# Performance work log

Measured on AMD Instinct MI355X. Metric: run time of the kernel, lower is better.

## Reference

```python
import jax, jax.numpy as jnp
import numpy as np

B, T, E, H, LBL = 32, 2048, 256, 256, 20


def _lstm_cell_step(x, W_ih, b_ih, b_hh):
    # Single LSTM cell step from zero state (h0=c0=0): W_hh @ h0 == 0.
    # x: [B, T, E]; W_ih: [4H, E]; gate order in torch: i, f, g, o
    gates = jnp.einsum('bte,ge->btg', x, W_ih) + b_ih + b_hh  # [B, T, 4H]
    i, f, g, o = jnp.split(gates, 4, axis=-1)
    c = jax.nn.sigmoid(i) * jnp.tanh(g)  # f * c0 == 0
    return jax.nn.sigmoid(o) * jnp.tanh(c)  # [B, T, H]


def setup_inputs() -> dict:
    key = jax.random.key(0)
    ks = jax.random.split(key, 12)
    s_ih = 1.0 / np.sqrt(H)
    inp = {
        'X': jax.random.normal(ks[0], (B, T, E), dtype=jnp.float32),
        'lengths': jax.random.randint(ks[1], (B,), 1, T + 1, dtype=jnp.int32),
        'W_ih_f': jax.random.uniform(ks[2], (4 * H, E), jnp.float32, -s_ih, s_ih),
        'b_ih_f': jax.random.uniform(ks[3], (4 * H,), jnp.float32, -s_ih, s_ih),
        'b_hh_f': jax.random.uniform(ks[4], (4 * H,), jnp.float32, -s_ih, s_ih),
        'W_ih_r': jax.random.uniform(ks[5], (4 * H, E), jnp.float32, -s_ih, s_ih),
        'b_ih_r': jax.random.uniform(ks[6], (4 * H,), jnp.float32, -s_ih, s_ih),
        'b_hh_r': jax.random.uniform(ks[7], (4 * H,), jnp.float32, -s_ih, s_ih),
        'W1': jax.random.uniform(ks[8], (256, 4 * H), jnp.float32, -1 / np.sqrt(4 * H), 1 / np.sqrt(4 * H)),
        'b1': jax.random.uniform(ks[9], (256,), jnp.float32, -1 / np.sqrt(4 * H), 1 / np.sqrt(4 * H)),
        'W2': jax.random.uniform(ks[10], (LBL, 256), jnp.float32, -1 / 16.0, 1 / 16.0),
        'b2': jax.random.uniform(ks[11], (LBL,), jnp.float32, -1 / 16.0, 1 / 16.0),
    }
    return inp


def reference(X, lengths, W_ih_f, b_ih_f, b_hh_f, W_ih_r, b_ih_r, b_hh_r, W1, b1, W2, b2):
    lengths = jnp.clip(lengths, 1, T).astype(jnp.int32)
    # Both directions are independent single-step cells (seq_len==1 in original)
    h_f = _lstm_cell_step(X, W_ih_f, b_ih_f, b_hh_f)  # [B, T, H]
    h_r = _lstm_cell_step(X, W_ih_r, b_ih_r, b_hh_r)  # [B, T, H]
    s = jnp.concatenate([h_f, h_r], axis=-1)          # [B, T, 2H]
    mask = (jnp.arange(T)[None, :] < lengths[:, None])  # [B, T]
    m = mask[:, :, None].astype(s.dtype)
    avg_pool = (s * m).sum(axis=1) / lengths[:, None].astype(s.dtype)  # [B, 2H]
    NEG = jnp.asarray(-1e30, s.dtype)
    max_pool = jnp.where(mask[:, :, None], s, NEG).max(axis=1)          # [B, 2H]
    doc = jnp.concatenate([avg_pool, max_pool], axis=-1)                # [B, 4H]
    rel = jax.nn.relu(doc)
    d1 = rel @ W1.T + b1        # dropout is identity in eval mode
    return d1 @ W2.T + b2        # [B, LBL]
```

## Files before the change

kernel.cpp:

```cpp
#include <hip/hip_runtime.h>
#include <stdint.h>

#define B_   32
#define T_   2048
#define E_   256
#define H_   256
#define LBL_ 20
#define M_   (B_ * T_)
#define NPACK_ 1536

typedef __attribute__((ext_vector_type(8))) short bf16x8;
typedef __attribute__((ext_vector_type(4))) float f32x4;

__device__ __forceinline__ unsigned short f2bf(float f) {
    union { float f; unsigned int u; } a; a.f = f;
    unsigned int u = a.u;
    u += 0x7FFFu + ((u >> 16) & 1u);
    return (unsigned short)(u >> 16);
}

__device__ __forceinline__ float rcp_(float x) {
#if __has_builtin(__builtin_amdgcn_rcpf)
    return __builtin_amdgcn_rcpf(x);
#else
    return 1.0f / x;
#endif
}
__device__ __forceinline__ float exp2_(float x) {
#if __has_builtin(__builtin_amdgcn_exp2f)
    return __builtin_amdgcn_exp2f(x);
#else
    return exp2f(x);
#endif
}

__global__ __launch_bounds__(256) void prep(
    const float4* __restrict__ X4, uint4* __restrict__ Xb4,
    const int* __restrict__ lengths,
    const float* __restrict__ Wf, const float* __restrict__ bif, const float* __restrict__ bhf,
    const float* __restrict__ Wr, const float* __restrict__ bir, const float* __restrict__ bhr,
    unsigned short* __restrict__ Wp, float* __restrict__ bias_p,
    int* __restrict__ live)
{
    int bi = blockIdx.x;
    if (bi < 8192) {
        int b = bi >> 8, tile = bi & 255;
        int lenb = lengths[b]; lenb = lenb < 1 ? 1 : (lenb > T_ ? T_ : lenb);
        int used = (lenb + 127) & ~127;
        if (tile * 8 >= used) return;
        int idx = b * 65536 + tile * 256 + threadIdx.x;
        float4 v0 = X4[2 * idx], v1 = X4[2 * idx + 1];
        union { unsigned short us[8]; uint4 u; } r;
        r.us[0] = f2bf(v0.x); r.us[1] = f2bf(v0.y); r.us[2] = f2bf(v0.z); r.us[3] = f2bf(v0.w);
        r.us[4] = f2bf(v1.x); r.us[5] = f2bf(v1.y); r.us[6] = f2bf(v1.z); r.us[7] = f2bf(v1.w);
        Xb4[idx] = r.u;
    } else if (bi < 8192 + NPACK_) {
        int n = bi - 8192, t = threadIdx.x;
        int gidx = n / 48, r = n % 48;
        int ty = r >> 4, cc = r & 15;
        int dir = gidx >> 4, c = (gidx & 15) * 16 + cc;
        int gate = (ty == 0) ? 0 : (ty == 1 ? 2 : 3);
        int wrow = gate * 256 + c;
        const float* W = dir ? Wr : Wf;
        Wp[n * 256 + t] = f2bf(W[wrow * 256 + t]);
        if (t == 0)
            bias_p[n] = (dir ? bir[wrow] : bif[wrow]) + (dir ? bhr[wrow] : bhf[wrow]);
    } else {
        __shared__ int cnts[32], offs[32], lens[32];
        int t = threadIdx.x;
        if (t < 32) {
            int lenb = lengths[t]; lenb = lenb < 1 ? 1 : (lenb > T_ ? T_ : lenb);
            lens[t] = lenb;
            cnts[t] = (lenb + 127) >> 7;
        }
        __syncthreads();
        if (t == 0) {
            int acc = 0;
            for (int b = 0; b < 32; ++b) { offs[b] = acc; acc += cnts[b]; }
            live[0] = acc;
        }
        __syncthreads();
        if (t < 32) {
            int o = offs[t], lenb = lens[t];
            for (int k = 0; k < cnts[t]; ++k)
                live[1 + o + k] = (lenb << 9) | (t * 16 + k);
        }
    }
}

__global__ __launch_bounds__(256, 3) void gemm_pool(
    const unsigned short* __restrict__ Xb, const unsigned short* __restrict__ Wp,
    const float* __restrict__ bias_p, const int* __restrict__ live,
    float* __restrict__ psum, float* __restrict__ pmax)
{
    __shared__ __align__(16) short Bs[96 * 256];
    __shared__ float red[2][4][2][16][2];

    const int tid    = threadIdx.x;
    const int w      = tid >> 6;
    const int lane   = tid & 63;
    const int n_tile = blockIdx.x / 48;
    const int worker = blockIdx.x % 48;
    const int n0     = n_tile * 96;
    const int q      = lane >> 4;
    const int cc     = lane & 15;

    #pragma unroll
    for (int rr = 0; rr < 12; ++rr) {
        int s = rr * 256 + tid;
        int row = s >> 5, kcs = s & 31;
        int kc = (kcs & 24) | ((kcs & 7) ^ (row & 7));
        __builtin_amdgcn_global_load_lds(
            (const __attribute__((address_space(1))) void*)(Wp + (n0 + row) * 256 + kc * 8),
            (__attribute__((address_space(3))) void*)(Bs + (rr * 256 + (w << 6)) * 8),
            16, 0, 0);
    }

    float bI[2], bG[2], bO[2];
    #pragma unroll
    for (int gg = 0; gg < 2; ++gg) {
        bI[gg] = bias_p[n0 + gg * 48 + 0  + cc];
        bG[gg] = bias_p[n0 + gg * 48 + 16 + cc];
        bO[gg] = bias_p[n0 + gg * 48 + 32 + cc];
    }

    const int nlive = live[0];
    const int* list = live + 1;

    int j = worker;
    int item = (j < nlive) ? list[j] : -1;
    const unsigned short* Ab = Xb;
    bf16x8 aU[4], aV[4];
    if (item >= 0) {
        Ab = Xb + (((item & 511) << 7) + w * 32 + (lane & 15)) * 256 + q * 8;
        #pragma unroll
        for (int ks = 0; ks < 2; ++ks)
            #pragma unroll
            for (int rt = 0; rt < 2; ++rt)
                aU[ks * 2 + rt] = *(const bf16x8*)(Ab + rt * 16 * 256 + ks * 4 * 8);
    }

    __syncthreads();

    int par = 0;
    const float L2E = 1.44269504f;

    while (item >= 0) {
        int jn = j + 48;
        int itemn = (jn < nlive) ? list[jn] : -1;
        const unsigned short* Abn = (itemn >= 0)
            ? Xb + (((itemn & 511) << 7) + w * 32 + (lane & 15)) * 256 + q * 8
            : Ab;

        f32x4 acc[2][6];
        #pragma unroll
        for (int i = 0; i < 2; ++i)
            #pragma unroll
            for (int jj = 0; jj < 6; ++jj) acc[i][jj] = (f32x4){0.f, 0.f, 0.f, 0.f};

        #pragma unroll
        for (int kit = 0; kit < 4; ++kit) {
            bf16x8* cur = (kit & 1) ? aV : aU;
            bf16x8* nxt = (kit & 1) ? aU : aV;
            if (kit < 3) {
                #pragma unroll
                for (int ks = 0; ks < 2; ++ks)
                    #pragma unroll
                    for (int rt = 0; rt < 2; ++rt)
                        nxt[ks * 2 + rt] = *(const bf16x8*)(Ab + rt * 16 * 256
                                                            + ((kit + 1) * 8 + ks * 4) * 8);
            } else {
                #pragma unroll
                for (int ks = 0; ks < 2; ++ks)
                    #pragma unroll
                    for (int rt = 0; rt < 2; ++rt)
                        nxt[ks * 2 + rt] = *(const bf16x8*)(Abn + rt * 16 * 256 + ks * 4 * 8);
            }
            #pragma unroll
            for (int ks = 0; ks < 2; ++ks) {
                bf16x8 bfr[6];
                int kc = kit * 8 + ks * 4 + q;
                #pragma unroll
                for (int ct = 0; ct < 6; ++ct) {
                    int rb = ct * 16 + (lane & 15);
                    int slot = rb * 32 + (kc & 24) + ((kc & 7) ^ (rb & 7));
                    bfr[ct] = *(const bf16x8*)(Bs + slot * 8);
                }
                #pragma unroll
                for (int rt = 0; rt < 2; ++rt)
                    #pragma unroll
                    for (int ct = 0; ct < 6; ++ct)
                        acc[rt][ct] = __builtin_amdgcn_mfma_f32_16x16x32_bf16(
                            cur[ks * 2 + rt], bfr[ct], acc[rt][ct], 0, 0, 0);
            }
        }

        const int idx9 = item & 511;
        const int lenb = item >> 9;
        const int t0   = (idx9 & 15) << 7;

        #pragma unroll
        for (int gg = 0; gg < 2; ++gg) {
            float hsum = 0.f, hmax = -1e30f;
            #pragma unroll
            for (int rt = 0; rt < 2; ++rt) {
                if (t0 + w * 32 + rt * 16 >= lenb) continue;
                #pragma unroll
                for (int reg = 0; reg < 4; ++reg) {
                    int row = w * 32 + rt * 16 + q * 4 + reg;
                    int t = t0 + row;
                    float iv = acc[rt][gg * 3 + 0][reg] + bI[gg];
                    float gv = acc[rt][gg * 3 + 1][reg] + bG[gg];
                    float ov = acc[rt][gg * 3 + 2][reg] + bO[gg];
                    float e1 = exp2_(iv * -L2E);
                    float e2 = exp2_(gv * -2.f * L2E);
                    float e3 = exp2_(ov * -L2E);
                    float cv = (1.f - e2) * rcp_((1.f + e1) * (1.f + e2));
                    float tt  = cv * cv;
                    float num = cv * __builtin_fmaf(tt, tt + 105.f, 945.f);
                    float den = __builtin_fmaf(tt, __builtin_fmaf(tt, 15.f, 420.f), 945.f);
                    float h = num * rcp_(den * (1.f + e3));
                    if (t < lenb) { hsum += h; hmax = fmaxf(hmax, h); }
                }
            }
            hsum += __shfl_xor(hsum, 16, 64);
            hmax = fmaxf(hmax, __shfl_xor(hmax, 16, 64));
            hsum += __shfl_xor(hsum, 32, 64);
            hmax = fmaxf(hmax, __shfl_xor(hmax, 32, 64));
            if (q == 0) { red[par][w][gg][cc][0] = hsum; red[par][w][gg][cc][1] = hmax; }
        }
        __syncthreads();
        if (tid < 32) {
            int gg = tid >> 4, c16 = tid & 15;
            float s  = red[par][0][gg][c16][0] + red[par][1][gg][c16][0]
                     + red[par][2][gg][c16][0] + red[par][3][gg][c16][0];
            float mx = fmaxf(fmaxf(red[par][0][gg][c16][1], red[par][1][gg][c16][1]),
                             fmaxf(red[par][2][gg][c16][1], red[par][3][gg][c16][1]));
            int gidx = n_tile * 2 + gg;
            int col2 = (gidx >> 4) * 256 + (gidx & 15) * 16 + c16;
            psum[idx9 * 512 + col2] = s;
            pmax[idx9 * 512 + col2] = mx;
        }
        par ^= 1;
        j = jn; item = itemn; Ab = Abn;
    }
}

__global__ __launch_bounds__(256) void mlp1(
    const float* __restrict__ psum, const float* __restrict__ pmax,
    const int* __restrict__ lengths,
    const float* __restrict__ W1, const float* __restrict__ b1,
    float* __restrict__ d1g)
{
    __shared__ float doc[1024];
    int nt = blockIdx.x, b = blockIdx.y, tid = threadIdx.x;
    int lenb = lengths[b]; lenb = lenb < 1 ? 1 : (lenb > T_ ? T_ : lenb);
    int cnt = (lenb + 127) >> 7;
    float invlen = 1.f / (float)lenb;
    for (int col = tid; col < 512; col += 256) {
        float s = 0.f, mx = -1e30f;
        for (int mt = 0; mt < cnt; ++mt) {
            s += psum[(b * 16 + mt) * 512 + col];
            mx = fmaxf(mx, pmax[(b * 16 + mt) * 512 + col]);
        }
        doc[col]       = fmaxf(s * invlen, 0.f);
        doc[512 + col] = fmaxf(mx, 0.f);
    }
    __syncthreads();
    int neuron = tid >> 2, tq = tid & 3;
    int row = nt * 64 + neuron;
    const float4* wrow = (const float4*)(W1 + row * 1024 + tq * 256);
    const float4* dv   = (const float4*)doc + tq * 64;
    float a0 = 0.f, a1 = 0.f, a2 = 0.f, a3 = 0.f;
    #pragma unroll 4
    for (int k = 0; k < 64; ++k) {
        float4 wv = wrow[k]; float4 xv = dv[k];
        a0 += wv.x * xv.x; a1 += wv.y * xv.y; a2 += wv.z * xv.z; a3 += wv.w * xv.w;
    }
    float a = a0 + a1 + a2 + a3;
    a += __shfl_xor(a, 1, 64);
    a += __shfl_xor(a, 2, 64);
    if (tq == 0) d1g[b * 256 + row] = a + b1[row];
}

__global__ __launch_bounds__(256) void mlp2(
    const float* __restrict__ d1g,
    const float* __restrict__ W2, const float* __restrict__ b2,
    float* __restrict__ out)
{
    __shared__ float d1s[256];
    int b = blockIdx.x, tid = threadIdx.x;
    d1s[tid] = d1g[b * 256 + tid];
    __syncthreads();
    int j = tid >> 3, tq = tid & 7;
    float a = 0.f;
    if (j < LBL_) {
        const float4* wr = (const float4*)(W2 + j * 256) + tq * 8;
        const float4* dd = (const float4*)d1s + tq * 8;
        #pragma unroll
        for (int k = 0; k < 8; ++k) {
            float4 wv = wr[k]; float4 xv = dd[k];
            a += wv.x * xv.x + wv.y * xv.y + wv.z * xv.z + wv.w * xv.w;
        }
    }
    a += __shfl_xor(a, 1, 64);
    a += __shfl_xor(a, 2, 64);
    a += __shfl_xor(a, 4, 64);
    if (j < LBL_ && tq == 0) out[b * LBL_ + j] = a + b2[j];
}

#define XB_OFF   0u
#define WP_OFF   33554432u
#define BIAS_OFF 34340864u
#define PSUM_OFF 34347008u
#define PMAX_OFF 35395584u
#define D1_OFF   36444160u
#define LIVE_OFF 36476928u

extern "C" void kernel_launch(void* const* d_in, const int* in_sizes, int n_in,
                              void* d_out, int out_size, void* d_ws, size_t ws_size,
                              hipStream_t stream) {
    (void)in_sizes; (void)n_in; (void)out_size; (void)ws_size;
    const float* X      = (const float*)d_in[0];
    const int*   lens   = (const int*)d_in[1];
    const float* W_ih_f = (const float*)d_in[2];
    const float* b_ih_f = (const float*)d_in[3];
    const float* b_hh_f = (const float*)d_in[4];
    const float* W_ih_r = (const float*)d_in[5];
    const float* b_ih_r = (const float*)d_in[6];
    const float* b_hh_r = (const float*)d_in[7];
    const float* W1     = (const float*)d_in[8];
    const float* b1     = (const float*)d_in[9];
    const float* W2     = (const float*)d_in[10];
    const float* b2     = (const float*)d_in[11];
    float* out = (float*)d_out;

    char* ws = (char*)d_ws;
    unsigned short* Xb     = (unsigned short*)(ws + XB_OFF);
    unsigned short* Wp     = (unsigned short*)(ws + WP_OFF);
    float*          bias_p = (float*)(ws + BIAS_OFF);
    float*          psum   = (float*)(ws + PSUM_OFF);
    float*          pmax   = (float*)(ws + PMAX_OFF);
    float*          d1g    = (float*)(ws + D1_OFF);
    int*            live   = (int*)(ws + LIVE_OFF);

    prep<<<dim3(8192 + NPACK_ + 1), 256, 0, stream>>>(
        (const float4*)X, (uint4*)Xb, lens,
        W_ih_f, b_ih_f, b_hh_f, W_ih_r, b_ih_r, b_hh_r, Wp, bias_p, live);
    gemm_pool<<<dim3(768), 256, 0, stream>>>(Xb, Wp, bias_p, live, psum, pmax);
    mlp1<<<dim3(4, 32), 256, 0, stream>>>(psum, pmax, lens, W1, b1, d1g);
    mlp2<<<dim3(B_), 256, 0, stream>>>(d1g, W2, b2, out);
}
```

Baseline: 177.6 us.

## Hold weight tile in registers, halve N-tile, drop LDS and A prefetch

The GEMM+pool kernel now uses 48-column N tiles (32 tiles by 24 workers, still 768 blocks). Each wave keeps its whole B fragment in registers, so the weight tile is no longer staged through shared memory. The A-operand double-buffer prefetch across items and k-steps is removed in favour of direct loads inside the k loop. The mlp1 kernel also splits its reduction over 8 lanes with twice as many blocks. The intent is to cut LDS traffic and raise parallelism, at the cost of re-reading shared weights per wave, higher register pressure, and losing the load/compute overlap.

```diff
diff --git a/kernel.cpp b/kernel.cpp
--- a/kernel.cpp
+++ b/kernel.cpp
@@ -93,156 +93,104 @@
     const float* __restrict__ bias_p, const int* __restrict__ live,
     float* __restrict__ psum, float* __restrict__ pmax)
 {
-    __shared__ __align__(16) short Bs[96 * 256];
-    __shared__ float red[2][4][2][16][2];
+    __shared__ float red[2][4][16][2];
 
     const int tid    = threadIdx.x;
     const int w      = tid >> 6;
     const int lane   = tid & 63;
-    const int n_tile = blockIdx.x / 48;
-    const int worker = blockIdx.x % 48;
-    const int n0     = n_tile * 96;
+    const int n_tile = blockIdx.x / 24;
+    const int worker = blockIdx.x % 24;
+    const int n0     = n_tile * 48;
     const int q      = lane >> 4;
     const int cc     = lane & 15;
 
+    bf16x8 bfr[3][8];
+    const unsigned short* Bb = Wp + (n0 + cc) * 256 + q * 8;
     #pragma unroll
-    for (int rr = 0; rr < 12; ++rr) {
-        int s = rr * 256 + tid;
-        int row = s >> 5, kcs = s & 31;
-        int kc = (kcs & 24) | ((kcs & 7) ^ (row & 7));
-        __builtin_amdgcn_global_load_lds(
-            (const __attribute__((address_space(1))) void*)(Wp + (n0 + row) * 256 + kc * 8),
-            (__attribute__((address_space(3))) void*)(Bs + (rr * 256 + (w << 6)) * 8),
-            16, 0, 0);
-    }
-
-    float bI[2], bG[2], bO[2];
-    #pragma unroll
-    for (int gg = 0; gg < 2; ++gg) {
-        bI[gg] = bias_p[n0 + gg * 48 + 0  + cc];
-        bG[gg] = bias_p[n0 + gg * 48 + 16 + cc];
-        bO[gg] = bias_p[n0 + gg * 48 + 32 + cc];
-    }
+    for (int ct = 0; ct < 3; ++ct)
+        #pragma unroll
+        for (int kk = 0; kk < 8; ++kk)
+            bfr[ct][kk] = *(const bf16x8*)(Bb + ct * 16 * 256
+                                           + ((kk >> 1) * 64 + (kk & 1) * 32));
+
+    const float bI = bias_p[n0 + 0  + cc];
+    const float bG = bias_p[n0 + 16 + cc];
+    const float bO = bias_p[n0 + 32 + cc];
 
     const int nlive = live[0];
     const int* list = live + 1;
+    const float L2E = 1.44269504f;
 
     int j = worker;
     int item = (j < nlive) ? list[j] : -1;
-    const unsigned short* Ab = Xb;
-    bf16x8 aU[4], aV[4];
-    if (item >= 0) {
-        Ab = Xb + (((item & 511) << 7) + w * 32 + (lane & 15)) * 256 + q * 8;
-        #pragma unroll
-        for (int ks = 0; ks < 2; ++ks)
-            #pragma unroll
-            for (int rt = 0; rt < 2; ++rt)
-                aU[ks * 2 + rt] = *(const bf16x8*)(Ab + rt * 16 * 256 + ks * 4 * 8);
-    }
-
-    __syncthreads();
-
     int par = 0;
-    const float L2E = 1.44269504f;
 
     while (item >= 0) {
-        int jn = j + 48;
-        int itemn = (jn < nlive) ? list[jn] : -1;
-        const unsigned short* Abn = (itemn >= 0)
-            ? Xb + (((itemn & 511) << 7) + w * 32 + (lane & 15)) * 256 + q * 8
-            : Ab;
-
-        f32x4 acc[2][6];
-        #pragma unroll
-        for (int i = 0; i < 2; ++i)
-            #pragma unroll
-            for (int jj = 0; jj < 6; ++jj) acc[i][jj] = (f32x4){0.f, 0.f, 0.f, 0.f};
-
-        #pragma unroll
-        for (int kit = 0; kit < 4; ++kit) {
-            bf16x8* cur = (kit & 1) ? aV : aU;
-            bf16x8* nxt = (kit & 1) ? aU : aV;
-            if (kit < 3) {
-                #pragma unroll
-                for (int ks = 0; ks < 2; ++ks)
-                    #pragma unroll
-                    for (int rt = 0; rt < 2; ++rt)
-                        nxt[ks * 2 + rt] = *(const bf16x8*)(Ab + rt * 16 * 256
-                                                            + ((kit + 1) * 8 + ks * 4) * 8);
-            } else {
-                #pragma unroll
-                for (int ks = 0; ks < 2; ++ks)
-                    #pragma unroll
-                    for (int rt = 0; rt < 2; ++rt)
-                        nxt[ks * 2 + rt] = *(const bf16x8*)(Abn + rt * 16 * 256 + ks * 4 * 8);
-            }
-            #pragma unroll
-            for (int ks = 0; ks < 2; ++ks) {
-                bf16x8 bfr[6];
-                int kc = kit * 8 + ks * 4 + q;
-                #pragma unroll
-                for (int ct = 0; ct < 6; ++ct) {
-                    int rb = ct * 16 + (lane & 15);
-                    int slot = rb * 32 + (kc & 24) + ((kc & 7) ^ (rb & 7));
-                    bfr[ct] = *(const bf16x8*)(Bs + slot * 8);
-                }
-                #pragma unroll
-                for (int rt = 0; rt < 2; ++rt)
-                    #pragma unroll
-                    for (int ct = 0; ct < 6; ++ct)
-                        acc[rt][ct] = __builtin_amdgcn_mfma_f32_16x16x32_bf16(
-                            cur[ks * 2 + rt], bfr[ct], acc[rt][ct], 0, 0, 0);
-            }
-        }
-
         const int idx9 = item & 511;
         const int lenb = item >> 9;
         const int t0   = (idx9 & 15) << 7;
-
-        #pragma unroll
-        for (int gg = 0; gg < 2; ++gg) {
-            float hsum = 0.f, hmax = -1e30f;
+        const unsigned short* Ab = Xb + ((idx9 << 7) + w * 32 + (lane & 15)) * 256 + q * 8;
+        const unsigned short* Ab1 = Ab + 16 * 256;
+
+        f32x4 acc[2][3];
+        #pragma unroll
+        for (int i = 0; i < 2; ++i)
             #pragma unroll
-            for (int rt = 0; rt < 2; ++rt) {
-                if (t0 + w * 32 + rt * 16 >= lenb) continue;
-                #pragma unroll
-                for (int reg = 0; reg < 4; ++reg) {
-                    int row = w * 32 + rt * 16 + q * 4 + reg;
-                    int t = t0 + row;
-                    float iv = acc[rt][gg * 3 + 0][reg] + bI[gg];
-                    float gv = acc[rt][gg * 3 + 1][reg] + bG[gg];
-                    float ov = acc[rt][gg * 3 + 2][reg] + bO[gg];
-                    float e1 = exp2_(iv * -L2E);
-                    float e2 = exp2_(gv * -2.f * L2E);
-                    float e3 = exp2_(ov * -L2E);
-                    float cv = (1.f - e2) * rcp_((1.f + e1) * (1.f + e2));
-                    float tt  = cv * cv;
-                    float num = cv * __builtin_fmaf(tt, tt + 105.f, 945.f);
-                    float den = __builtin_fmaf(tt, __builtin_fmaf(tt, 15.f, 420.f), 945.f);
-                    float h = num * rcp_(den * (1.f + e3));
-                    if (t < lenb) { hsum += h; hmax = fmaxf(hmax, h); }
-                }
+            for (int c = 0; c < 3; ++c) acc[i][c] = (f32x4){0.f, 0.f, 0.f, 0.f};
+
+        #pragma unroll
+        for (int kk = 0; kk < 8; ++kk) {
+            int ko = (kk >> 1) * 64 + (kk & 1) * 32;
+            bf16x8 a0 = *(const bf16x8*)(Ab  + ko);
+            bf16x8 a1 = *(const bf16x8*)(Ab1 + ko);
+            #pragma unroll
+            for (int ct = 0; ct < 3; ++ct) {
+                acc[0][ct] = __builtin_amdgcn_mfma_f32_16x16x32_bf16(
+                    a0, bfr[ct][kk], acc[0][ct], 0, 0, 0);
+                acc[1][ct] = __builtin_amdgcn_mfma_f32_16x16x32_bf16(
+                    a1, bfr[ct][kk], acc[1][ct], 0, 0, 0);
             }
-            hsum += __shfl_xor(hsum, 16, 64);
-            hmax = fmaxf(hmax, __shfl_xor(hmax, 16, 64));
-            hsum += __shfl_xor(hsum, 32, 64);
-            hmax = fmaxf(hmax, __shfl_xor(hmax, 32, 64));
-            if (q == 0) { red[par][w][gg][cc][0] = hsum; red[par][w][gg][cc][1] = hmax; }
-        }
+        }
+
+        float hsum = 0.f, hmax = -1e30f;
+        #pragma unroll
+        for (int rt = 0; rt < 2; ++rt) {
+            if (t0 + w * 32 + rt * 16 >= lenb) continue;
+            #pragma unroll
+            for (int reg = 0; reg < 4; ++reg) {
+                int t = t0 + w * 32 + rt * 16 + q * 4 + reg;
+                float iv = acc[rt][0][reg] + bI;
+                float gv = acc[rt][1][reg] + bG;
+                float ov = acc[rt][2][reg] + bO;
+                float e1 = exp2_(iv * -L2E);
+                float e2 = exp2_(gv * -2.f * L2E);
+                float e3 = exp2_(ov * -L2E);
+                float cv = (1.f - e2) * rcp_((1.f + e1) * (1.f + e2));
+                float tt  = cv * cv;
+                float num = cv * __builtin_fmaf(tt, tt + 105.f, 945.f);
+                float den = __builtin_fmaf(tt, __builtin_fmaf(tt, 15.f, 420.f), 945.f);
+                float h = num * rcp_(den * (1.f + e3));
+                if (t < lenb) { hsum += h; hmax = fmaxf(hmax, h); }
+            }
+        }
+        hsum += __shfl_xor(hsum, 16, 64);
+        hmax = fmaxf(hmax, __shfl_xor(hmax, 16, 64));
+        hsum += __shfl_xor(hsum, 32, 64);
+        hmax = fmaxf(hmax, __shfl_xor(hmax, 32, 64));
+        if (q == 0) { red[par][w][cc][0] = hsum; red[par][w][cc][1] = hmax; }
         __syncthreads();
-        if (tid < 32) {
-            int gg = tid >> 4, c16 = tid & 15;
-            float s  = red[par][0][gg][c16][0] + red[par][1][gg][c16][0]
-                     + red[par][2][gg][c16][0] + red[par][3][gg][c16][0];
-            float mx = fmaxf(fmaxf(red[par][0][gg][c16][1], red[par][1][gg][c16][1]),
-                             fmaxf(red[par][2][gg][c16][1], red[par][3][gg][c16][1]));
-            int gidx = n_tile * 2 + gg;
-            int col2 = (gidx >> 4) * 256 + (gidx & 15) * 16 + c16;
+        if (tid < 16) {
+            float s  = red[par][0][tid][0] + red[par][1][tid][0]
+                     + red[par][2][tid][0] + red[par][3][tid][0];
+            float mx = fmaxf(fmaxf(red[par][0][tid][1], red[par][1][tid][1]),
+                             fmaxf(red[par][2][tid][1], red[par][3][tid][1]));
+            int col2 = (n_tile >> 4) * 256 + (n_tile & 15) * 16 + tid;
             psum[idx9 * 512 + col2] = s;
             pmax[idx9 * 512 + col2] = mx;
         }
         par ^= 1;
-        j = jn; item = itemn; Ab = Abn;
+        j += 24;
+        item = (j < nlive) ? list[j] : -1;
     }
 }
 
@@ -267,20 +215,21 @@
         doc[512 + col] = fmaxf(mx, 0.f);
     }
     __syncthreads();
-    int neuron = tid >> 2, tq = tid & 3;
-    int row = nt * 64 + neuron;
-    const float4* wrow = (const float4*)(W1 + row * 1024 + tq * 256);
-    const float4* dv   = (const float4*)doc + tq * 64;
+    int neuron = tid >> 3, tk = tid & 7;
+    int row = nt * 32 + neuron;
+    const float4* wrow = (const float4*)(W1 + row * 1024 + tk * 128);
+    const float4* dv   = (const float4*)doc + tk * 32;
     float a0 = 0.f, a1 = 0.f, a2 = 0.f, a3 = 0.f;
     #pragma unroll 4
-    for (int k = 0; k < 64; ++k) {
+    for (int k = 0; k < 32; ++k) {
         float4 wv = wrow[k]; float4 xv = dv[k];
         a0 += wv.x * xv.x; a1 += wv.y * xv.y; a2 += wv.z * xv.z; a3 += wv.w * xv.w;
     }
     float a = a0 + a1 + a2 + a3;
     a += __shfl_xor(a, 1, 64);
     a += __shfl_xor(a, 2, 64);
-    if (tq == 0) d1g[b * 256 + row] = a + b1[row];
+    a += __shfl_xor(a, 4, 64);
+    if (tk == 0) d1g[b * 256 + row] = a + b1[row];
 }
 
 __global__ __launch_bounds__(256) void mlp2(
@@ -348,6 +297,6 @@
         (const float4*)X, (uint4*)Xb, lens,
         W_ih_f, b_ih_f, b_hh_f, W_ih_r, b_ih_r, b_hh_r, Wp, bias_p, live);
     gemm_pool<<<dim3(768), 256, 0, stream>>>(Xb, Wp, bias_p, live, psum, pmax);
-    mlp1<<<dim3(4, 32), 256, 0, stream>>>(psum, pmax, lens, W1, b1, d1g);
+    mlp1<<<dim3(8, 32), 256, 0, stream>>>(psum, pmax, lens, W1, b1, d1g);
     mlp2<<<dim3(B_), 256, 0, stream>>>(d1g, W2, b2, out);
 }
```

New measurement: 204.3 us. +15.0%, slower.
